# Kernel optimization log

Measured on AMD Instinct MI355X. Metric: run time of the kernel, lower is better.

Reference implementation:

```python
import jax, jax.numpy as jnp
import numpy as np

N_NODES = 4096
F_UAV = 64
N_OBS = N_NODES * F_UAV + 256  # 262400
H = 1024
N_ACT = 64
N_EDGES = 65536


def setup_inputs() -> dict:
    key = jax.random.key(0)
    ks = jax.random.split(key, 13)
    s = lambda fan_in: 1.0 / np.sqrt(fan_in)
    return {
        "node_x": jax.random.normal(ks[0], (N_NODES, F_UAV), jnp.float32),
        "flat_obs": jax.random.normal(ks[1], (N_OBS,), jnp.float32),
        "gcn_w": jax.random.normal(ks[2], (F_UAV, F_UAV), jnp.float32) * s(F_UAV),
        "gcn_b": jnp.zeros((F_UAV,), jnp.float32),
        "w1": jax.random.normal(ks[3], (N_OBS, H), jnp.float32) * s(N_OBS),
        "b1": jnp.zeros((H,), jnp.float32),
        "w2": jax.random.normal(ks[4], (H, H), jnp.float32) * s(H),
        "b2": jnp.zeros((H,), jnp.float32),
        "wv": jax.random.normal(ks[5], (H, 1), jnp.float32) * s(H),
        "bv": jnp.zeros((1,), jnp.float32),
        "wa": jax.random.normal(ks[6], (H, N_ACT), jnp.float32) * s(H),
        "ba": jnp.zeros((N_ACT,), jnp.float32),
        "edge_index": jax.random.randint(ks[7], (2, N_EDGES), 0, N_NODES, jnp.int64),
    }


def _gcn_conv(x, edge_index, w, b):
    n = x.shape[0]
    loops = jnp.arange(n, dtype=edge_index.dtype)
    src = jnp.concatenate([edge_index[0], loops])
    dst = jnp.concatenate([edge_index[1], loops])
    deg = jax.ops.segment_sum(jnp.ones_like(dst, dtype=x.dtype), dst, num_segments=n)
    dinv = jax.lax.rsqrt(deg)  # deg >= 1 thanks to self-loops
    norm = dinv[src] * dinv[dst]          # [E+N]
    h = x @ w                              # [N, F]
    msg = h[src] * norm[:, None]           # gather + scale
    out = jax.ops.segment_sum(msg, dst, num_segments=n)  # scatter-add
    return out + b


def reference(node_x, flat_obs, gcn_w, gcn_b, w1, b1, w2, b2, wv, bv, wa, ba, edge_index):
    y_uav = _gcn_conv(node_x, edge_index, gcn_w, gcn_b).reshape(-1)  # flatten
    x = jnp.concatenate([y_uav, flat_obs[y_uav.shape[0]:]], axis=0)  # [N_OBS]
    y = jax.nn.relu(x @ w1 + b1)
    y = jax.nn.relu(y @ w2 + b2)
    value = y @ wv + bv                    # [1]
    adv = y @ wa + ba                      # [N_ACT]
    return value + adv - jnp.mean(adv, keepdims=True)
```

## Files before the change

kernel.cpp:

```cpp
#include <hip/hip_runtime.h>

#define N_NODES 4096
#define F_UAV 64
#define NOBS 262400
#define GCN_FLAT (N_NODES * F_UAV)
#define HDIM 1024
#define N_ACT 64
#define N_EDGES 65536

typedef float f32x4 __attribute__((ext_vector_type(4)));

#define MV1_GRID 2048
#define MV1_BIGN 256
#define MV1_BIG 129
#define MV1_SMALL 128

#define OFF_X      0
#define OFF_H      262400
#define OFF_DINV   (OFF_H + GCN_FLAT)
#define OFF_DEG    (OFF_DINV + N_NODES)
#define OFF_BASE   (OFF_DEG + N_NODES)
#define OFF_CUR    (OFF_BASE + N_NODES)
#define OFF_SSRC   (OFF_CUR + N_NODES)
#define OFF_P1     (OFF_SSRC + N_EDGES)
#define OFF_Q1     (OFF_P1 + 2048*1024)
#define OFF_Y1     (OFF_Q1 + 128*1024)
#define OFF_P2     (OFF_Y1 + HDIM)
#define OFF_Q2     (OFF_P2 + 256*1024)

__global__ __launch_bounds__(256) void k_gcn_h(const float* __restrict__ nx,
                                               const float* __restrict__ w,
                                               float* __restrict__ h,
                                               int* __restrict__ deg) {
    __shared__ float sw[F_UAV * F_UAV];
    __shared__ float sx4[256];
    int tid = threadIdx.x;
    if (blockIdx.x < 16) deg[blockIdx.x * 256 + tid] = 0;
    for (int i = tid; i < F_UAV * F_UAV; i += 256) sw[i] = w[i];
    sx4[tid] = nx[blockIdx.x * 256 + tid];
    __syncthreads();
    int r = tid >> 6, j = tid & 63;
    float acc = 0.f;
#pragma unroll
    for (int k = 0; k < F_UAV; ++k) acc += sx4[r * 64 + k] * sw[k * F_UAV + j];
    h[blockIdx.x * 256 + r * 64 + j] = acc;
}

__global__ void k_deg_count(const int* __restrict__ dst, int* deg) {
    int e = blockIdx.x * 256 + threadIdx.x;
    if (e < N_EDGES) atomicAdd(&deg[dst[e]], 1);
}

__global__ __launch_bounds__(1024) void k_prefix(const int* __restrict__ deg,
                                                 int* __restrict__ base,
                                                 int* __restrict__ cursor,
                                                 float* __restrict__ dinv,
                                                 const float* __restrict__ obs,
                                                 float* __restrict__ x) {
    __shared__ int ssum[1024];
    int t = threadIdx.x;
    int d0 = deg[4 * t], d1 = deg[4 * t + 1], d2 = deg[4 * t + 2], d3 = deg[4 * t + 3];
    int local = d0 + d1 + d2 + d3;
    ssum[t] = local;
    __syncthreads();
    for (int off = 1; off < 1024; off <<= 1) {
        int v = (t >= off) ? ssum[t - off] : 0;
        __syncthreads();
        ssum[t] += v;
        __syncthreads();
    }
    int excl = ssum[t] - local;
    int b0 = excl, b1 = b0 + d0, b2 = b1 + d1, b3 = b2 + d2;
    base[4 * t] = b0;     cursor[4 * t] = b0;
    base[4 * t + 1] = b1; cursor[4 * t + 1] = b1;
    base[4 * t + 2] = b2; cursor[4 * t + 2] = b2;
    base[4 * t + 3] = b3; cursor[4 * t + 3] = b3;
    dinv[4 * t]     = rsqrtf((float)(d0 + 1));
    dinv[4 * t + 1] = rsqrtf((float)(d1 + 1));
    dinv[4 * t + 2] = rsqrtf((float)(d2 + 1));
    dinv[4 * t + 3] = rsqrtf((float)(d3 + 1));
    if (t < NOBS - GCN_FLAT) x[GCN_FLAT + t] = obs[GCN_FLAT + t];
}

__global__ void k_place(const int* __restrict__ src, const int* __restrict__ dst,
                        int* __restrict__ cursor, int* __restrict__ ssrc) {
    int e = blockIdx.x * 256 + threadIdx.x;
    if (e < N_EDGES) {
        int slot = atomicAdd(&cursor[dst[e]], 1);
        ssrc[slot] = src[e];
    }
}

__global__ __launch_bounds__(256) void k_gather(const int* __restrict__ base,
                                                const int* __restrict__ deg,
                                                const int* __restrict__ ssrc,
                                                const float* __restrict__ h,
                                                const float* __restrict__ dinv,
                                                const float* __restrict__ gb,
                                                float* __restrict__ x) {
    int tid = threadIdx.x;
    int n = blockIdx.x * 4 + (tid >> 6);
    int j = tid & 63;
    int lo = base[n], cnt = deg[n];
    int end = lo + cnt;
    float acc0 = 0.f, acc1 = 0.f;
    int i = lo;
    for (; i + 1 < end; i += 2) {
        int s0 = ssrc[i], s1 = ssrc[i + 1];
        acc0 += h[s0 * 64 + j] * dinv[s0];
        acc1 += h[s1 * 64 + j] * dinv[s1];
    }
    if (i < end) {
        int s = ssrc[i];
        acc0 += h[s * 64 + j] * dinv[s];
    }
    float dn = dinv[n];
    x[n * 64 + j] = (acc0 + acc1) * dn + h[n * 64 + j] * dn * dn + gb[j];
}

__global__ __launch_bounds__(256) void k_matvec(const float* __restrict__ x,
                                                const float* __restrict__ W,
                                                float* __restrict__ part,
                                                int big_n, int big_sz, int small_sz) {
    __shared__ float sx[132];
    int tid = threadIdx.x;
    int b = blockIdx.x;
    int k0 = (b < big_n) ? b * big_sz : big_n * big_sz + (b - big_n) * small_sz;
    int cnt = (b < big_n) ? big_sz : small_sz;
    for (int i = tid; i < cnt; i += 256) sx[i] = x[k0 + i];
    __syncthreads();
    f32x4 acc = {0.f, 0.f, 0.f, 0.f};
    const f32x4* Wr = ((const f32x4*)W) + (size_t)k0 * (HDIM / 4) + tid;
    int kk = cnt & ~7;
    int k = 0;
    for (; k < kk; k += 8) {
#pragma unroll
        for (int u = 0; u < 8; ++u) {
            float xv = sx[k + u];
            f32x4 w = Wr[(size_t)(k + u) * (HDIM / 4)];
            acc += xv * w;
        }
    }
    for (; k < cnt; ++k) acc += sx[k] * Wr[(size_t)k * (HDIM / 4)];
    ((f32x4*)(part + (size_t)b * HDIM))[tid] = acc;
}

__global__ __launch_bounds__(256) void k_sum16(const float* __restrict__ part,
                                               float* __restrict__ q) {
    int t = threadIdx.x, s = blockIdx.x;
    const f32x4* p = ((const f32x4*)part) + (size_t)s * 16 * (HDIM / 4) + t;
    f32x4 acc = {0.f, 0.f, 0.f, 0.f};
#pragma unroll
    for (int r = 0; r < 16; ++r) acc += p[(size_t)r * (HDIM / 4)];
    ((f32x4*)q)[(size_t)s * (HDIM / 4) + t] = acc;
}

__global__ void k_finish128(const float* __restrict__ q, const float* __restrict__ b,
                            float* __restrict__ y) {
    int j = blockIdx.x * 256 + threadIdx.x;
    float acc = b[j];
#pragma unroll 8
    for (int s = 0; s < 128; ++s) acc += q[s * HDIM + j];
    y[j] = fmaxf(acc, 0.f);
}

__global__ __launch_bounds__(1024) void k_heads_f(const float* __restrict__ q2,
                                                  const float* __restrict__ b2,
                                                  const float* __restrict__ wv,
                                                  const float* __restrict__ bv,
                                                  const float* __restrict__ wa,
                                                  const float* __restrict__ ba,
                                                  float* __restrict__ out) {
    __shared__ float y2s[1024];
    __shared__ float s_adv[16][64];
    __shared__ float s_pv[1024];
    int t = threadIdx.x;
    float acc = b2[t];
#pragma unroll
    for (int s = 0; s < 16; ++s) acc += q2[s * HDIM + t];
    float y = fmaxf(acc, 0.f);
    y2s[t] = y;
    s_pv[t] = y * wv[t];
    __syncthreads();
    int g = t >> 6, a = t & 63;
    float pa = 0.f;
#pragma unroll 4
    for (int kk = 0; kk < 64; ++kk) pa += y2s[g * 64 + kk] * wa[(g * 64 + kk) * 64 + a];
    s_adv[g][a] = pa;
    __syncthreads();
    if (t < 64) {
        float adv = ba[a];
#pragma unroll
        for (int gg = 0; gg < 16; ++gg) adv += s_adv[gg][a];
        float v = 0.f;
#pragma unroll
        for (int i = 0; i < 16; ++i) v += s_pv[a + 64 * i];
        for (int off = 32; off; off >>= 1) v += __shfl_xor(v, off);
        float m = adv;
        for (int off = 32; off; off >>= 1) m += __shfl_xor(m, off);
        m *= (1.f / 64.f);
        out[a] = (v + bv[0]) + adv - m;
    }
}

extern "C" void kernel_launch(void* const* d_in, const int* in_sizes, int n_in,
                              void* d_out, int out_size, void* d_ws, size_t ws_size,
                              hipStream_t stream) {
    const float* node_x   = (const float*)d_in[0];
    const float* flat_obs = (const float*)d_in[1];
    const float* gcn_w    = (const float*)d_in[2];
    const float* gcn_b    = (const float*)d_in[3];
    const float* w1       = (const float*)d_in[4];
    const float* b1       = (const float*)d_in[5];
    const float* w2       = (const float*)d_in[6];
    const float* b2       = (const float*)d_in[7];
    const float* wv       = (const float*)d_in[8];
    const float* bv       = (const float*)d_in[9];
    const float* wa       = (const float*)d_in[10];
    const float* ba       = (const float*)d_in[11];
    const int*   ei       = (const int*)d_in[12];
    const int* src = ei;
    const int* dst = ei + N_EDGES;

    float* ws   = (float*)d_ws;
    float* x    = ws + OFF_X;
    float* h    = ws + OFF_H;
    float* dinv = ws + OFF_DINV;
    int*   deg  = (int*)(ws + OFF_DEG);
    int*   base = (int*)(ws + OFF_BASE);
    int*   cur  = (int*)(ws + OFF_CUR);
    int*   ssrc = (int*)(ws + OFF_SSRC);
    float* p1   = ws + OFF_P1;
    float* q1   = ws + OFF_Q1;
    float* y1   = ws + OFF_Y1;
    float* p2   = ws + OFF_P2;
    float* q2   = ws + OFF_Q2;
    float* out  = (float*)d_out;

    k_gcn_h<<<N_NODES / 4, 256, 0, stream>>>(node_x, gcn_w, h, deg);
    k_deg_count<<<N_EDGES / 256, 256, 0, stream>>>(dst, deg);
    k_prefix<<<1, 1024, 0, stream>>>(deg, base, cur, dinv, flat_obs, x);
    k_place<<<N_EDGES / 256, 256, 0, stream>>>(src, dst, cur, ssrc);
    k_gather<<<N_NODES / 4, 256, 0, stream>>>(base, deg, ssrc, h, dinv, gcn_b, x);

    k_matvec<<<MV1_GRID, 256, 0, stream>>>(x, w1, p1, MV1_BIGN, MV1_BIG, MV1_SMALL);
    k_sum16<<<128, 256, 0, stream>>>(p1, q1);
    k_finish128<<<4, 256, 0, stream>>>(q1, b1, y1);

    k_matvec<<<256, 256, 0, stream>>>(y1, w2, p2, 256, 4, 4);
    k_sum16<<<16, 256, 0, stream>>>(p2, q2);
    k_heads_f<<<1, 1024, 0, stream>>>(q2, b2, wv, bv, wa, ba, out);
}
```

Before: 258.2 us.

## Fuse degree counting into GCN kernel, fold layer-1 finish into layer-2 matvec, nontemporal W1 loads

Degree counting is merged into the GCN feature-transform kernel, and deg is zeroed with a memset, which removes one launch. The layer-1 reduction now writes its partial sums transposed, so a new kernel can finish y1 (bias plus ReLU through a wave reduction) and compute its slice of the W2 matvec in the same launch. This replaces the separate finish128 kernel and the second matvec. The streaming W1 loads use nontemporal hints to limit cache pollution, and the transposed stores are strided, which may cost some write efficiency.

```diff
diff --git a/kernel.cpp b/kernel.cpp
--- a/kernel.cpp
+++ b/kernel.cpp
@@ -9,6 +9,7 @@
 #define N_EDGES 65536
 
 typedef float f32x4 __attribute__((ext_vector_type(4)));
+typedef float f32x2 __attribute__((ext_vector_type(2)));
 
 #define MV1_GRID 2048
 #define MV1_BIGN 256
@@ -23,32 +24,27 @@
 #define OFF_CUR    (OFF_BASE + N_NODES)
 #define OFF_SSRC   (OFF_CUR + N_NODES)
 #define OFF_P1     (OFF_SSRC + N_EDGES)
-#define OFF_Q1     (OFF_P1 + 2048*1024)
-#define OFF_Y1     (OFF_Q1 + 128*1024)
-#define OFF_P2     (OFF_Y1 + HDIM)
-#define OFF_Q2     (OFF_P2 + 256*1024)
+#define OFF_Q1T    (OFF_P1 + 2048*1024)
+#define OFF_P2     (OFF_Q1T + 1024*128)
+#define OFF_Q2T    (OFF_P2 + 256*1024)
 
 __global__ __launch_bounds__(256) void k_gcn_h(const float* __restrict__ nx,
                                                const float* __restrict__ w,
+                                               const int* __restrict__ dst,
                                                float* __restrict__ h,
                                                int* __restrict__ deg) {
     __shared__ float sw[F_UAV * F_UAV];
     __shared__ float sx4[256];
     int tid = threadIdx.x;
-    if (blockIdx.x < 16) deg[blockIdx.x * 256 + tid] = 0;
     for (int i = tid; i < F_UAV * F_UAV; i += 256) sw[i] = w[i];
     sx4[tid] = nx[blockIdx.x * 256 + tid];
+    if (blockIdx.x < 256) atomicAdd(&deg[dst[blockIdx.x * 256 + tid]], 1);
     __syncthreads();
     int r = tid >> 6, j = tid & 63;
     float acc = 0.f;
 #pragma unroll
     for (int k = 0; k < F_UAV; ++k) acc += sx4[r * 64 + k] * sw[k * F_UAV + j];
     h[blockIdx.x * 256 + r * 64 + j] = acc;
-}
-
-__global__ void k_deg_count(const int* __restrict__ dst, int* deg) {
-    int e = blockIdx.x * 256 + threadIdx.x;
-    if (e < N_EDGES) atomicAdd(&deg[dst[e]], 1);
 }
 
 __global__ __launch_bounds__(1024) void k_prefix(const int* __restrict__ deg,
@@ -137,34 +133,47 @@
 #pragma unroll
         for (int u = 0; u < 8; ++u) {
             float xv = sx[k + u];
-            f32x4 w = Wr[(size_t)(k + u) * (HDIM / 4)];
+            f32x4 w = __builtin_nontemporal_load(&Wr[(size_t)(k + u) * (HDIM / 4)]);
             acc += xv * w;
         }
     }
-    for (; k < cnt; ++k) acc += sx[k] * Wr[(size_t)k * (HDIM / 4)];
+    for (; k < cnt; ++k) acc += sx[k] * __builtin_nontemporal_load(&Wr[(size_t)k * (HDIM / 4)]);
     ((f32x4*)(part + (size_t)b * HDIM))[tid] = acc;
 }
 
-__global__ __launch_bounds__(256) void k_sum16(const float* __restrict__ part,
-                                               float* __restrict__ q) {
+template <int NSEG>
+__global__ __launch_bounds__(256) void k_sum16T(const float* __restrict__ part,
+                                                float* __restrict__ qT) {
     int t = threadIdx.x, s = blockIdx.x;
     const f32x4* p = ((const f32x4*)part) + (size_t)s * 16 * (HDIM / 4) + t;
     f32x4 acc = {0.f, 0.f, 0.f, 0.f};
 #pragma unroll
     for (int r = 0; r < 16; ++r) acc += p[(size_t)r * (HDIM / 4)];
-    ((f32x4*)q)[(size_t)s * (HDIM / 4) + t] = acc;
-}
-
-__global__ void k_finish128(const float* __restrict__ q, const float* __restrict__ b,
-                            float* __restrict__ y) {
-    int j = blockIdx.x * 256 + threadIdx.x;
-    float acc = b[j];
-#pragma unroll 8
-    for (int s = 0; s < 128; ++s) acc += q[s * HDIM + j];
-    y[j] = fmaxf(acc, 0.f);
-}
-
-__global__ __launch_bounds__(1024) void k_heads_f(const float* __restrict__ q2,
+#pragma unroll
+    for (int u = 0; u < 4; ++u) qT[(size_t)(4 * t + u) * NSEG + s] = acc[u];
+}
+
+__global__ __launch_bounds__(256) void k_fin_mv2(const float* __restrict__ q1T,
+                                                 const float* __restrict__ b1,
+                                                 const float* __restrict__ w2,
+                                                 float* __restrict__ p2) {
+    __shared__ float s_y[4];
+    int t = threadIdx.x, b = blockIdx.x;
+    int w = t >> 6, l = t & 63;
+    int j = 4 * b + w;
+    f32x2 v = *(const f32x2*)&q1T[(size_t)j * 128 + 2 * l];
+    float sm = v.x + v.y;
+    for (int off = 32; off; off >>= 1) sm += __shfl_xor(sm, off);
+    if (l == 0) s_y[w] = fmaxf(b1[j] + sm, 0.f);
+    __syncthreads();
+    f32x4 acc = {0.f, 0.f, 0.f, 0.f};
+    const f32x4* Wr = ((const f32x4*)w2) + (size_t)(4 * b) * (HDIM / 4) + t;
+#pragma unroll
+    for (int i = 0; i < 4; ++i) acc += s_y[i] * Wr[(size_t)i * (HDIM / 4)];
+    ((f32x4*)(p2 + (size_t)b * HDIM))[t] = acc;
+}
+
+__global__ __launch_bounds__(1024) void k_heads_f(const float* __restrict__ q2T,
                                                   const float* __restrict__ b2,
                                                   const float* __restrict__ wv,
                                                   const float* __restrict__ bv,
@@ -177,7 +186,7 @@
     int t = threadIdx.x;
     float acc = b2[t];
 #pragma unroll
-    for (int s = 0; s < 16; ++s) acc += q2[s * HDIM + t];
+    for (int s = 0; s < 16; ++s) acc += q2T[t * 16 + s];
     float y = fmaxf(acc, 0.f);
     y2s[t] = y;
     s_pv[t] = y * wv[t];
@@ -231,23 +240,20 @@
     int*   cur  = (int*)(ws + OFF_CUR);
     int*   ssrc = (int*)(ws + OFF_SSRC);
     float* p1   = ws + OFF_P1;
-    float* q1   = ws + OFF_Q1;
-    float* y1   = ws + OFF_Y1;
+    float* q1T  = ws + OFF_Q1T;
     float* p2   = ws + OFF_P2;
-    float* q2   = ws + OFF_Q2;
+    float* q2T  = ws + OFF_Q2T;
     float* out  = (float*)d_out;
 
-    k_gcn_h<<<N_NODES / 4, 256, 0, stream>>>(node_x, gcn_w, h, deg);
-    k_deg_count<<<N_EDGES / 256, 256, 0, stream>>>(dst, deg);
+    hipMemsetAsync(deg, 0, N_NODES * sizeof(int), stream);
+    k_gcn_h<<<N_NODES / 4, 256, 0, stream>>>(node_x, gcn_w, dst, h, deg);
     k_prefix<<<1, 1024, 0, stream>>>(deg, base, cur, dinv, flat_obs, x);
     k_place<<<N_EDGES / 256, 256, 0, stream>>>(src, dst, cur, ssrc);
     k_gather<<<N_NODES / 4, 256, 0, stream>>>(base, deg, ssrc, h, dinv, gcn_b, x);
 
     k_matvec<<<MV1_GRID, 256, 0, stream>>>(x, w1, p1, MV1_BIGN, MV1_BIG, MV1_SMALL);
-    k_sum16<<<128, 256, 0, stream>>>(p1, q1);
-    k_finish128<<<4, 256, 0, stream>>>(q1, b1, y1);
-
-    k_matvec<<<256, 256, 0, stream>>>(y1, w2, p2, 256, 4, 4);
-    k_sum16<<<16, 256, 0, stream>>>(p2, q2);
-    k_heads_f<<<1, 1024, 0, stream>>>(q2, b2, wv, bv, wa, ba, out);
-}
+    k_sum16T<128><<<128, 256, 0, stream>>>(p1, q1T);
+    k_fin_mv2<<<256, 256, 0, stream>>>(q1T, b1, w2, p2);
+    k_sum16T<16><<<16, 256, 0, stream>>>(p2, q2T);
+    k_heads_f<<<1, 1024, 0, stream>>>(q2T, b2, wv, bv, wa, ba, out);
+}
```

Measured after the change: 230.1 us. 10.9% less time.
